# Kernel optimization log

Measured on AMD Instinct MI355X. Metric: run time of the kernel, lower is better.

The kernel has to match this reference:

```python
import jax, jax.numpy as jnp
import numpy as np

A = 16          # n_agents
H = 128         # rnn_hidden_dim
IN = 128        # input_shape
NA = 32         # n_attention
NACT = 14       # n_actions
TAU = 0.5       # gumbel_softmax_tau
B_ENV = 1024    # parallel envs
BZ = B_ENV * A

# neighbor index: for agent i, all j != i (matches select_ind in torch code)
IDX = np.array([[j for j in range(A) if j != i] for i in range(A)])  # [A, A-1]


def gru_cell(x, h, Wih, Whh, bih, bhh):
    # torch GRUCell gate order: r, z, n
    gi = x @ Wih.T + bih
    gh = h @ Whh.T + bhh
    ir, iz, inn = jnp.split(gi, 3, axis=-1)
    hr, hz, hn = jnp.split(gh, 3, axis=-1)
    r = jax.nn.sigmoid(ir + hr)
    z = jax.nn.sigmoid(iz + hz)
    n = jnp.tanh(inn + r * hn)
    return (1.0 - z) * n + z * h


def run_gru(seq, Wih, Whh, bih, bhh):
    # seq: [T, N, D]; returns all hidden states [T, N, H]
    h0 = jnp.zeros((seq.shape[1], Whh.shape[1]), seq.dtype)
    def step(h, x):
        h2 = gru_cell(x, h, Wih, Whh, bih, bhh)
        return h2, h2
    _, ys = jax.lax.scan(step, h0, seq)
    return ys


def setup_inputs() -> dict:
    key = jax.random.key(0)
    ks = jax.random.split(key, 24)
    def u(k, shape, fan):
        s = 1.0 / np.sqrt(fan)
        return jax.random.uniform(k, shape, jnp.float32, -s, s)
    inp = {
        "inputs": jax.random.normal(ks[0], (BZ, IN), jnp.float32),
        "hidden_state": jax.random.normal(ks[1], (BZ, H), jnp.float32),
        "gumbel_u": jax.random.uniform(ks[2], (BZ * (A - 1), 2), jnp.float32),
        # fc1
        "W1": u(ks[3], (H, IN), IN), "b1": u(ks[4], (H,), IN),
        # GRUCell
        "Wih_c": u(ks[5], (3 * H, H), H), "Whh_c": u(ks[6], (3 * H, H), H),
        "bih_c": u(ks[7], (3 * H,), H), "bhh_c": u(ks[8], (3 * H,), H),
        # bi-GRU forward dir (input 2H)
        "Wih_f": u(ks[9], (3 * H, 2 * H), H), "Whh_f": u(ks[10], (3 * H, H), H),
        "bih_f": u(ks[11], (3 * H,), H), "bhh_f": u(ks[12], (3 * H,), H),
        # bi-GRU backward dir
        "Wih_b": u(ks[13], (3 * H, 2 * H), H), "Whh_b": u(ks[14], (3 * H, H), H),
        "bih_b": u(ks[15], (3 * H,), H), "bhh_b": u(ks[16], (3 * H,), H),
        # hard classifier
        "Wc": u(ks[17], (2, 2 * H), 2 * H), "bc": u(ks[18], (2,), 2 * H),
        # attention projections (no bias)
        "Wq": u(ks[19], (NA, H), H), "Wk": u(ks[20], (NA, H), H),
        # fc2
        "W2": u(ks[21], (NACT, 2 * H), 2 * H), "b2": u(ks[22], (NACT,), 2 * H),
    }
    return inp


def reference(inputs, hidden_state, gumbel_u, W1, b1, Wih_c, Whh_c, bih_c, bhh_c,
              Wih_f, Whh_f, bih_f, bhh_f, Wih_b, Whh_b, bih_b, bhh_b,
              Wc, bc, Wq, Wk, W2, b2):
    bz = inputs.shape[0]
    B = bz // A
    x1 = jax.nn.relu(inputs @ W1.T + b1)
    h_rnn = gru_cell(x1, hidden_state.reshape(-1, H), Wih_c, Whh_c, bih_c, bhh_c)  # [bz, H]

    h3 = h_rnn.reshape(B, A, H)
    nbr = h3[:, IDX, :]                                           # [B, A, A-1, H]
    self_rep = jnp.broadcast_to(h3[:, :, None, :], (B, A, A - 1, H))
    pairs = jnp.concatenate([self_rep, nbr], axis=-1)             # [B, A, A-1, 2H]
    seq = pairs.transpose(2, 0, 1, 3).reshape(A - 1, bz, 2 * H)   # [T, bz, 2H]

    yf = run_gru(seq, Wih_f, Whh_f, bih_f, bhh_f)
    yb = jnp.flip(run_gru(jnp.flip(seq, 0), Wih_b, Whh_b, bih_b, bhh_b), 0)
    h_hard = jnp.concatenate([yf, yb], axis=-1)                   # [T, bz, 2H]
    h_hard = h_hard.transpose(1, 0, 2).reshape(-1, 2 * H)         # [bz*T, 2H]

    logits = h_hard @ Wc.T + bc                                   # [bz*T, 2]
    g = -jnp.log(-jnp.log(gumbel_u + 1e-10) + 1e-10)
    gs = jax.nn.softmax((logits + g) / TAU, axis=-1)
    hard_w = gs[:, 1].reshape(B, A, A - 1)                        # hard gate

    q = (h_rnn @ Wq.T).reshape(B, A, NA)
    k = (h_rnn @ Wk.T).reshape(B, A, NA)
    kn = k[:, IDX, :] * hard_w[..., None]                         # [B, A, A-1, NA]
    scores = jnp.einsum('bad,bamd->bam', q, kn) / np.sqrt(NA)
    soft_w = jax.nn.softmax(scores, axis=-1)                      # [B, A, A-1]

    w = hard_w * soft_w
    agg = jnp.einsum('bam,bamh->bah', w, nbr).reshape(bz, H)
    out = jnp.concatenate([h_rnn, agg], axis=-1) @ W2.T + b2      # [bz, n_actions]
    return out, h_rnn
```

## Files before the change

### kernel.cpp

```cpp
#include <hip/hip_runtime.h>
#include <hip/hip_bf16.h>


typedef __attribute__((ext_vector_type(8))) short short8;
typedef __attribute__((ext_vector_type(4))) short short4v;
typedef __attribute__((ext_vector_type(4))) float float4v;

#define BF2F(x) __bfloat162float(x)
typedef __hip_bfloat16 bf;

__device__ __forceinline__ float frcp(float x) {
  return __builtin_amdgcn_rcpf(x);
}
__device__ __forceinline__ float fsigmoid(float x) {
  return frcp(1.f + __expf(-x));
}
__device__ __forceinline__ float ftanh(float x) {
  float e = __expf(2.f * x);
  return 1.f - 2.f * frcp(1.f + e);
}
__device__ __forceinline__ float rdv(const void* p, int i, int f) {
  return f ? ((const float*)p)[i] : BF2F(((const bf*)p)[i]);
}

static const int AO[23] = {
  0, 2097152, 4194304, 4685824, 4702208, 4702336, 4751488, 4800640, 4801024,
  4801408, 4899712, 4948864, 4949248, 4949632, 5047936, 5097088, 5097472,
  5097856, 5098368, 5098384, 5102480, 5106576, 5110160};
static const int AN[23] = {
  2097152, 2097152, 491520, 16384, 128, 49152, 49152, 384, 384, 98304, 49152,
  384, 384, 98304, 49152, 384, 384, 512, 2, 4096, 4096, 3584, 14};

struct CArgs {
  const void* src[23];
  int n[23];
  int off[23];
};

__global__ void kConvert(CArgs a, int* __restrict__ flagOut,
                         bf* __restrict__ arena,
                         const void* __restrict__ WqR, const void* __restrict__ WkR,
                         const void* __restrict__ W2R, const void* __restrict__ WcR,
                         bf* __restrict__ Wqk, bf* __restrict__ W2p,
                         bf* __restrict__ Wcb) {
  __shared__ int sflag;
  if (threadIdx.x == 0) sflag = 0;
  __syncthreads();
  {
    const unsigned short* p0 = (const unsigned short*)a.src[0];
    int hit = 0;
    for (int i = threadIdx.x; i < 4096; i += 256) {
      int e = (p0[i] >> 7) & 0xFF;
      if (e >= 0xC0) hit = 1;
    }
    if (hit) atomicOr(&sflag, 1);
  }
  __syncthreads();
  const int f = sflag;
  const int b = blockIdx.y;
  if (b == 0 && blockIdx.x == 0 && threadIdx.x == 0) *flagOut = f;

  if (b == 23) {
    int idx = blockIdx.x * 256 + threadIdx.x;
    if (idx < 8192) {
      int r = idx >> 7, c = idx & 127;
      float v = (r < 32) ? rdv(WqR, r * 128 + c, f) : rdv(WkR, (r - 32) * 128 + c, f);
      Wqk[idx] = __float2bfloat16(v);
    }
    if (idx < 4096)
      W2p[idx] = __float2bfloat16((idx < 3584) ? rdv(W2R, idx, f) : 0.f);
    if (idx < 512) {
      int dir = idx >> 8, l = (idx >> 7) & 1, k = idx & 127;
      Wcb[idx] = __float2bfloat16(rdv(WcR, l * 256 + dir * 128 + k, f));
    }
    return;
  }
  if (b == 2 || b == 18 || b == 22) return;
  const int n = a.n[b];
  const int nv = n & ~7;
  bf* dst = arena + a.off[b];
  const int gid = blockIdx.x * 256 + threadIdx.x;
  const int gs = gridDim.x * 256;
  if (f) {
    const float* s = (const float*)a.src[b];
    for (int i = gid * 8; i < nv; i += gs * 8) {
      float4 x0 = *(const float4*)(s + i);
      float4 x1 = *(const float4*)(s + i + 4);
      short8 v;
      bf t;
      t = __float2bfloat16(x0.x); v[0] = *(short*)&t;
      t = __float2bfloat16(x0.y); v[1] = *(short*)&t;
      t = __float2bfloat16(x0.z); v[2] = *(short*)&t;
      t = __float2bfloat16(x0.w); v[3] = *(short*)&t;
      t = __float2bfloat16(x1.x); v[4] = *(short*)&t;
      t = __float2bfloat16(x1.y); v[5] = *(short*)&t;
      t = __float2bfloat16(x1.z); v[6] = *(short*)&t;
      t = __float2bfloat16(x1.w); v[7] = *(short*)&t;
      *(short8*)(dst + i) = v;
    }
    for (int i = nv + gid; i < n; i += gs) dst[i] = __float2bfloat16(s[i]);
  } else {
    const short8* s = (const short8*)a.src[b];
    short8* d = (short8*)dst;
    for (int i = gid; i * 8 < nv; i += gs) d[i] = s[i];
    const unsigned short* ss = (const unsigned short*)a.src[b];
    unsigned short* ds = (unsigned short*)dst;
    for (int i = nv + gid; i < n; i += gs) ds[i] = ss[i];
  }
}

__global__ __launch_bounds__(256) void kFused12(
    const bf* __restrict__ inputs, const bf* __restrict__ W1,
    const bf* __restrict__ b1, const bf* __restrict__ Wih,
    const bf* __restrict__ bih, bf* __restrict__ gi) {
  __shared__ bf sX[16][136];
  const int tid = threadIdx.x;
  const int wave = tid >> 6, lane = tid & 63;
  const int quad = lane >> 4, ci = lane & 15;
  const int row0 = blockIdx.x * 16;

  float4v xa[2];
#pragma unroll
  for (int i = 0; i < 2; ++i) xa[i] = {0.f, 0.f, 0.f, 0.f};
#pragma unroll
  for (int ks = 0; ks < 4; ++ks) {
    short8 inr = *(const short8*)(inputs + (size_t)(row0 + ci) * 128 + ks * 32 + quad * 8);
#pragma unroll
    for (int c2 = 0; c2 < 2; ++c2) {
      int ct = wave * 2 + c2;
      short8 wfr = *(const short8*)(W1 + (size_t)(ct * 16 + ci) * 128 + ks * 32 + quad * 8);
      xa[c2] = __builtin_amdgcn_mfma_f32_16x16x32_bf16(wfr, inr, xa[c2], 0, 0, 0);
    }
  }
#pragma unroll
  for (int c2 = 0; c2 < 2; ++c2) {
    int ct = wave * 2 + c2;
    short4v v4;
#pragma unroll
    for (int r = 0; r < 4; ++r) {
      float v = xa[c2][r] + BF2F(b1[ct * 16 + quad * 4 + r]);
      v = fmaxf(v, 0.f);
      bf t = __float2bfloat16(v);
      v4[r] = *(short*)&t;
    }
    *(short4v*)&sX[ci][ct * 16 + quad * 4] = v4;
  }
  __syncthreads();

  short8 af[4];
#pragma unroll
  for (int ks = 0; ks < 4; ++ks)
    af[ks] = *(const short8*)&sX[ci][ks * 32 + quad * 8];

  float4v acc[6];
#pragma unroll
  for (int i = 0; i < 6; ++i) acc[i] = {0.f, 0.f, 0.f, 0.f};
#pragma unroll
  for (int ks = 0; ks < 4; ++ks)
#pragma unroll
    for (int j = 0; j < 6; ++j) {
      short8 b = *(const short8*)(Wih + (size_t)((wave * 6 + j) * 16 + ci) * 128 + ks * 32 + quad * 8);
      acc[j] = __builtin_amdgcn_mfma_f32_16x16x32_bf16(af[ks], b, acc[j], 0, 0, 0);
    }
#pragma unroll
  for (int j = 0; j < 6; ++j) {
    int col = (wave * 6 + j) * 16 + ci;
    float bv = BF2F(bih[col]);
#pragma unroll
    for (int r = 0; r < 4; ++r)
      gi[(size_t)(row0 + quad * 4 + r) * 384 + col] = __float2bfloat16(acc[j][r] + bv);
  }
}

__global__ __launch_bounds__(256, 4) void kStep(
    const bf* __restrict__ Hp, const bf* __restrict__ Whh,
    const bf* __restrict__ G, int gld,
    const bf* __restrict__ bhh,
    bf* __restrict__ Ho, float* __restrict__ HcopyF) {
  const int half = blockIdx.z;
  const int tid = threadIdx.x;
  const int wave = tid >> 6, lane = tid & 63;
  const int quad = lane >> 4, ci = lane & 15;
  const int mr = blockIdx.x * 32 + (wave & 1) * 16;
  const int nt0 = (wave >> 1) * 2;

  float4v acc[6];
#pragma unroll
  for (int i = 0; i < 6; ++i) acc[i] = {0.f, 0.f, 0.f, 0.f};

#pragma unroll
  for (int ks = 0; ks < 4; ++ks) {
    short8 a = *(const short8*)(Hp + (size_t)(mr + ci) * 128 + ks * 32 + quad * 8);
#pragma unroll
    for (int g = 0; g < 3; ++g)
#pragma unroll
      for (int nt = 0; nt < 2; ++nt) {
        short8 b = *(const short8*)(Whh + (size_t)(g * 128 + half * 64 + (nt0 + nt) * 16 + ci) * 128 + ks * 32 + quad * 8);
        acc[g * 2 + nt] = __builtin_amdgcn_mfma_f32_16x16x32_bf16(a, b, acc[g * 2 + nt], 0, 0, 0);
      }
  }

  float bR[2], bZ[2], bN[2];
#pragma unroll
  for (int nt = 0; nt < 2; ++nt) {
    int c = half * 64 + (nt0 + nt) * 16 + ci;
    bR[nt] = BF2F(bhh[c]);
    bZ[nt] = BF2F(bhh[128 + c]);
    bN[nt] = BF2F(bhh[256 + c]);
  }

#pragma unroll
  for (int r = 0; r < 4; ++r) {
    int rr = mr + quad * 4 + r;
    const bf* gs = G + (size_t)rr * gld;
#pragma unroll
    for (int nt = 0; nt < 2; ++nt) {
      int c = half * 64 + (nt0 + nt) * 16 + ci;
      float gr = BF2F(gs[c]), gz = BF2F(gs[128 + c]), gnn = BF2F(gs[256 + c]);
      float pre_r = acc[nt][r] + gr + bR[nt];
      float pre_z = acc[2 + nt][r] + gz + bZ[nt];
      float hn_   = acc[4 + nt][r] + bN[nt];
      float rg = fsigmoid(pre_r);
      float zg = fsigmoid(pre_z);
      float ng = ftanh(gnn + rg * hn_);
      float hp = BF2F(Hp[(size_t)rr * 128 + c]);
      float hv = ng + zg * (hp - ng);
      Ho[(size_t)rr * 128 + c] = __float2bfloat16(hv);
      if (HcopyF) HcopyF[(size_t)rr * 128 + c] = hv;
    }
  }
}

__global__ __launch_bounds__(512, 4) void kSeq(
    const bf* __restrict__ hrnn,
    const bf* __restrict__ Wih_f, const bf* __restrict__ Wih_b,
    const bf* __restrict__ Whh_f, const bf* __restrict__ Whh_b,
    const bf* __restrict__ bih_f, const bf* __restrict__ bih_b,
    const bf* __restrict__ bhh_f, const bf* __restrict__ bhh_b,
    const bf* __restrict__ Wcb, float* __restrict__ L) {
  __shared__ float sGiN[16][3][132];
  __shared__ bf sH[2][16][136];
  __shared__ float sL[16][15][2];
  __shared__ bf sWc[2][136];

  const int env = blockIdx.x;
  const int dir = blockIdx.y;
  const int tid = threadIdx.x;
  const int wave = tid >> 6, lane = tid & 63;
  const int nh = wave;
  const int quad = lane >> 4, ci = lane & 15;
  const bf* Wih = dir ? Wih_b : Wih_f;
  const bf* Whh = dir ? Whh_b : Whh_f;
  const bf* bih = dir ? bih_b : bih_f;
  const bf* bhh = dir ? bhh_b : bhh_f;
  const int h0q = nh * 16 + quad * 4;

  float4v gS[3], gN[3];
#pragma unroll
  for (int i = 0; i < 3; ++i) { gS[i] = {0.f, 0.f, 0.f, 0.f}; gN[i] = {0.f, 0.f, 0.f, 0.f}; }
#pragma unroll
  for (int ks = 0; ks < 4; ++ks) {
    short8 bh = *(const short8*)(hrnn + (size_t)(env * 16 + ci) * 128 + ks * 32 + quad * 8);
#pragma unroll
    for (int g = 0; g < 3; ++g) {
      const bf* wrow = Wih + (size_t)(g * 128 + nh * 16 + ci) * 256 + ks * 32 + quad * 8;
      short8 ws = *(const short8*)(wrow);
      short8 wn = *(const short8*)(wrow + 128);
      gS[g] = __builtin_amdgcn_mfma_f32_16x16x32_bf16(ws, bh, gS[g], 0, 0, 0);
      gN[g] = __builtin_amdgcn_mfma_f32_16x16x32_bf16(wn, bh, gN[g], 0, 0, 0);
    }
  }
#pragma unroll
  for (int g = 0; g < 3; ++g)
#pragma unroll
    for (int r = 0; r < 4; ++r) {
      int c = g * 128 + h0q + r;
      float bv = BF2F(bih[c]);
      if (g < 2) bv += BF2F(bhh[c]);
      gS[g][r] += bv;
    }
#pragma unroll
  for (int g = 0; g < 3; ++g)
    *(float4v*)&sGiN[ci][g][h0q] = gN[g];

  {
    bf z = __float2bfloat16(0.f);
    bf* p = &sH[0][0][0];
    for (int i = tid; i < 16 * 136; i += 512) p[i] = z;
    if (tid < 256)
      sWc[tid >> 7][tid & 127] = Wcb[(dir * 2 + (tid >> 7)) * 128 + (tid & 127)];
  }

  short8 Bf[12];
#pragma unroll
  for (int g = 0; g < 3; ++g)
#pragma unroll
    for (int ks = 0; ks < 4; ++ks)
      Bf[g * 4 + ks] =
          *(const short8*)(Whh + (size_t)(g * 128 + nh * 16 + ci) * 128 + ks * 32 + quad * 8);

  float bNc[4];
#pragma unroll
  for (int r = 0; r < 4; ++r) bNc[r] = BF2F(bhh[256 + h0q + r]);

  float hPrev[4];
#pragma unroll
  for (int r = 0; r < 4; ++r) hPrev[r] = 0.f;

  __syncthreads();

  for (int t = 0; t < 15; ++t) {
    const int cur = t & 1, nxt = cur ^ 1;
    const int m = dir ? (14 - t) : t;
    const int jr = m + ((m >= ci) ? 1 : 0);

    float4v nbR = *(const float4v*)&sGiN[jr][0][h0q];
    float4v nbZ = *(const float4v*)&sGiN[jr][1][h0q];
    float4v nbN = *(const float4v*)&sGiN[jr][2][h0q];

    float4v acc[3];
#pragma unroll
    for (int i = 0; i < 3; ++i) acc[i] = {0.f, 0.f, 0.f, 0.f};
    float4v lacc = {0.f, 0.f, 0.f, 0.f};
#pragma unroll
    for (int ks = 0; ks < 4; ++ks) {
      short8 bh = *(const short8*)&sH[cur][ci][ks * 32 + quad * 8];
#pragma unroll
      for (int g = 0; g < 3; ++g)
        acc[g] = __builtin_amdgcn_mfma_f32_16x16x32_bf16(Bf[g * 4 + ks], bh, acc[g], 0, 0, 0);
      if (nh == 0) {
        short8 wv = *(const short8*)&sWc[ci & 1][ks * 32 + quad * 8];
        lacc = __builtin_amdgcn_mfma_f32_16x16x32_bf16(wv, bh, lacc, 0, 0, 0);
      }
    }
    if (nh == 0 && t > 0 && quad == 0) {
      int mp = dir ? (15 - t) : (t - 1);
      sL[ci][mp][0] = lacc[0];
      sL[ci][mp][1] = lacc[1];
    }

    short4v hv4;
#pragma unroll
    for (int r = 0; r < 4; ++r) {
      float pre_r = acc[0][r] + gS[0][r] + nbR[r];
      float pre_z = acc[1][r] + gS[1][r] + nbZ[r];
      float gnn   = gS[2][r] + nbN[r];
      float hn_   = acc[2][r] + bNc[r];
      float rg = fsigmoid(pre_r);
      float zg = fsigmoid(pre_z);
      float ng = ftanh(gnn + rg * hn_);
      float hv = ng + zg * (hPrev[r] - ng);
      hPrev[r] = hv;
      bf b = __float2bfloat16(hv);
      hv4[r] = *(short*)&b;
    }
    *(short4v*)&sH[nxt][ci][h0q] = hv4;
    __syncthreads();
  }

  if (nh == 0) {
    float4v lacc = {0.f, 0.f, 0.f, 0.f};
#pragma unroll
    for (int ks = 0; ks < 4; ++ks) {
      short8 bh = *(const short8*)&sH[1][ci][ks * 32 + quad * 8];
      short8 wv = *(const short8*)&sWc[ci & 1][ks * 32 + quad * 8];
      lacc = __builtin_amdgcn_mfma_f32_16x16x32_bf16(wv, bh, lacc, 0, 0, 0);
    }
    if (quad == 0) {
      int mf = dir ? 0 : 14;
      sL[ci][mf][0] = lacc[0];
      sL[ci][mf][1] = lacc[1];
    }
  }
  __syncthreads();

  {
    float* Ld = L + (size_t)dir * 491520 + (size_t)env * 480;
    for (int i = tid; i < 480; i += 512) {
      int row = i / 30, rem = i - row * 30;
      int mm = rem >> 1, l = rem & 1;
      Ld[i] = sL[row][mm][l];
    }
  }
}

__global__ __launch_bounds__(256) void kTail(
    const bf* __restrict__ h, const bf* __restrict__ Wqk,
    const float* __restrict__ L, const void* __restrict__ guRaw,
    const void* __restrict__ bcRaw, const int* __restrict__ flag,
    const bf* __restrict__ W2p, const void* __restrict__ b2Raw,
    float* __restrict__ out) {
  __shared__ float sh[16 * 132];
  __shared__ float sqk[16 * 64];
  __shared__ float shw[240];
  __shared__ float sw[16 * 16];
  __shared__ bf sAgg[16][136];
  const int bb = blockIdx.x;
  const int tid = threadIdx.x;
  const int f = *flag;
  const int a = tid >> 4, i = tid & 15;

  {
    const int w = tid >> 6, lane = tid & 63;
    const int quad = lane >> 4, ci = lane & 15;
    float4v acc = {0.f, 0.f, 0.f, 0.f};
#pragma unroll
    for (int ks = 0; ks < 4; ++ks) {
      short8 a_ = *(const short8*)(h + (size_t)(bb * 16 + ci) * 128 + ks * 32 + quad * 8);
      short8 b_ = *(const short8*)(Wqk + (size_t)(w * 16 + ci) * 128 + ks * 32 + quad * 8);
      acc = __builtin_amdgcn_mfma_f32_16x16x32_bf16(a_, b_, acc, 0, 0, 0);
    }
#pragma unroll
    for (int r = 0; r < 4; ++r)
      sqk[(quad * 4 + r) * 64 + w * 16 + ci] = acc[r];
  }
  for (int k = tid; k < 2048; k += 256)
    sh[(k >> 7) * 132 + (k & 127)] = BF2F(h[(size_t)bb * 2048 + k]);
  if (tid < 240) {
    int idx = bb * 240 + tid;
    float l0 = L[(size_t)idx * 2]     + L[491520 + (size_t)idx * 2]     + rdv(bcRaw, 0, f);
    float l1 = L[(size_t)idx * 2 + 1] + L[491520 + (size_t)idx * 2 + 1] + rdv(bcRaw, 1, f);
    float u0 = rdv(guRaw, idx * 2, f);
    float u1 = rdv(guRaw, idx * 2 + 1, f);
    float g0 = -__logf(-__logf(u0 + 1e-10f) + 1e-10f);
    float g1 = -__logf(-__logf(u1 + 1e-10f) + 1e-10f);
    shw[tid] = fsigmoid(((l1 + g1) - (l0 + g0)) * 2.0f);
  }
  __syncthreads();

  float s = -1e30f;
  if (i < 15) {
    int j = i + (i >= a);
    float d = 0.f;
#pragma unroll
    for (int c = 0; c < 32; ++c) d += sqk[a * 64 + c] * sqk[j * 64 + 32 + c];
    s = shw[a * 15 + i] * d * 0.17677669529663687f;
  }
  float mx = s;
#pragma unroll
  for (int d = 1; d < 16; d <<= 1) mx = fmaxf(mx, __shfl_xor(mx, d));
  float ex = (i < 15) ? __expf(s - mx) : 0.f;
  float sum = ex;
#pragma unroll
  for (int d = 1; d < 16; d <<= 1) sum += __shfl_xor(sum, d);
  float w = (i < 15) ? (ex * frcp(sum)) * shw[a * 15 + i] : 0.f;
  sw[a * 16 + i] = w;
  __syncthreads();

  float ac[8] = {0, 0, 0, 0, 0, 0, 0, 0};
  for (int mm = 0; mm < 15; ++mm) {
    int jm = mm + (mm >= a);
    float wm = sw[a * 16 + mm];
    const float* shp = &sh[jm * 132 + i * 8];
    float4 h0 = *(const float4*)shp;
    float4 h1 = *(const float4*)(shp + 4);
    ac[0] += wm * h0.x; ac[1] += wm * h0.y; ac[2] += wm * h0.z; ac[3] += wm * h0.w;
    ac[4] += wm * h1.x; ac[5] += wm * h1.y; ac[6] += wm * h1.z; ac[7] += wm * h1.w;
  }
  short8 v;
#pragma unroll
  for (int d = 0; d < 8; ++d) {
    bf b = __float2bfloat16(ac[d]);
    v[d] = *(short*)&b;
  }
  *(short8*)&sAgg[a][i * 8] = v;
  __syncthreads();

  if (tid < 64) {
    const int quad = tid >> 4, ci = tid & 15;
    const int mr = bb * 16;
    float4v acc = {0.f, 0.f, 0.f, 0.f};
#pragma unroll
    for (int ks = 0; ks < 4; ++ks) {
      short8 a_ = *(const short8*)(h + (size_t)(mr + ci) * 128 + ks * 32 + quad * 8);
      short8 b_ = *(const short8*)(W2p + (size_t)ci * 256 + ks * 32 + quad * 8);
      acc = __builtin_amdgcn_mfma_f32_16x16x32_bf16(a_, b_, acc, 0, 0, 0);
    }
#pragma unroll
    for (int ks = 0; ks < 4; ++ks) {
      short8 a_ = *(const short8*)&sAgg[ci][ks * 32 + quad * 8];
      short8 b_ = *(const short8*)(W2p + (size_t)ci * 256 + 128 + ks * 32 + quad * 8);
      acc = __builtin_amdgcn_mfma_f32_16x16x32_bf16(a_, b_, acc, 0, 0, 0);
    }
    if (ci < 14) {
      float bv = rdv(b2Raw, ci, f);
#pragma unroll
      for (int r = 0; r < 4; ++r)
        out[(size_t)(mr + quad * 4 + r) * 14 + ci] = acc[r] + bv;
    }
  }
}

extern "C" void kernel_launch(void* const* d_in, const int* in_sizes, int n_in,
                              void* d_out, int out_size, void* d_ws, size_t ws_size,
                              hipStream_t stream) {
  const size_t OFF_ARENA = 0;
  const size_t OFF_FLAG  = 10220544;
  const size_t OFF_A     = 10220800;
  const size_t OFF_WQK   = 26998016;
  const size_t OFF_WCB   = 27014400;
  const size_t OFF_W2P   = 27410944;
  const size_t OFF_HRNN  = 27419136;
  const size_t NEEDED    = 84042240;
  if (ws_size < NEEDED) return;
  if (n_in < 23 || in_sizes[0] != 2097152 || in_sizes[3] != 16384 ||
      in_sizes[5] != 49152 || in_sizes[9] != 98304 || in_sizes[17] != 512 ||
      in_sizes[19] != 4096 || in_sizes[21] != 3584 || out_size != 2326528)
    return;

  char* ws = (char*)d_ws;
  bf*    arena = (bf*)(ws + OFF_ARENA);
  float* L     = (float*)(ws + OFF_ARENA);
  int*   flag  = (int*)(ws + OFF_FLAG);
  bf*    gi_c  = (bf*)(ws + OFF_A + 4194304);
  bf*    Wqk   = (bf*)(ws + OFF_WQK);
  bf*    Wcb   = (bf*)(ws + OFF_WCB);
  bf*    W2p   = (bf*)(ws + OFF_W2P);
  bf*    hrnn  = (bf*)(ws + OFF_HRNN);

  float* out14 = (float*)d_out;
  float* outh  = (float*)d_out + 229376;

  CArgs ca;
  for (int i = 0; i < 23; ++i) { ca.src[i] = d_in[i]; ca.n[i] = AN[i]; ca.off[i] = AO[i]; }
  kConvert<<<dim3(128, 24), 256, 0, stream>>>(ca, flag, arena,
                                              d_in[19], d_in[20], d_in[21], d_in[17],
                                              Wqk, W2p, Wcb);

  const bf* inputs = arena + AO[0];
  const bf* hidden = arena + AO[1];
  const bf* W1     = arena + AO[3];
  const bf* b1     = arena + AO[4];
  const bf* Wih_c  = arena + AO[5];
  const bf* Whh_c  = arena + AO[6];
  const bf* bih_c  = arena + AO[7];
  const bf* bhh_c  = arena + AO[8];
  const bf* Wih_f  = arena + AO[9];
  const bf* Whh_f  = arena + AO[10];
  const bf* bih_f  = arena + AO[11];
  const bf* bhh_f  = arena + AO[12];
  const bf* Wih_b  = arena + AO[13];
  const bf* Whh_b  = arena + AO[14];
  const bf* bih_b  = arena + AO[15];
  const bf* bhh_b  = arena + AO[16];

  kFused12<<<dim3(1024), 256, 0, stream>>>(inputs, W1, b1, Wih_c, bih_c, gi_c);
  kStep<<<dim3(512, 1, 2), 256, 0, stream>>>(hidden, Whh_c, gi_c, 384, bhh_c,
                                             hrnn, outh);
  kSeq<<<dim3(1024, 2), 512, 0, stream>>>(hrnn, Wih_f, Wih_b, Whh_f, Whh_b,
                                          bih_f, bih_b, bhh_f, bhh_b, Wcb, L);
  kTail<<<dim3(1024), 256, 0, stream>>>(hrnn, Wqk, L, d_in[2], d_in[18], flag,
                                        W2p, d_in[22], out14);
}
```

Baseline: 267.4 us.

## Fuse fc1, GRU input projection and GRU cell step into one kernel

Merges the fc1+Wih kernel and the GRUCell step kernel into a single kernel. Each block now computes both the input and hidden gate projections with MFMA and applies the gate math in registers. This removes the bf16 gi intermediate round trip through global memory and one kernel launch. Separately, the sequence kernel now seeds its MFMA accumulators with the precomputed gate and bias terms, saving a few adds per step. The fused kernel keeps twelve accumulators per wave instead of six, which raises register pressure.

```diff
diff --git a/kernel.cpp b/kernel.cpp
--- a/kernel.cpp
+++ b/kernel.cpp
@@ -109,10 +109,12 @@
   }
 }
 
-__global__ __launch_bounds__(256) void kFused12(
+__global__ __launch_bounds__(256) void kPre(
     const bf* __restrict__ inputs, const bf* __restrict__ W1,
     const bf* __restrict__ b1, const bf* __restrict__ Wih,
-    const bf* __restrict__ bih, bf* __restrict__ gi) {
+    const bf* __restrict__ bih, const bf* __restrict__ hidden,
+    const bf* __restrict__ Whh, const bf* __restrict__ bhh,
+    bf* __restrict__ hrnn, float* __restrict__ outh) {
   __shared__ bf sX[16][136];
   const int tid = threadIdx.x;
   const int wave = tid >> 6, lane = tid & 63;
@@ -152,81 +154,44 @@
   for (int ks = 0; ks < 4; ++ks)
     af[ks] = *(const short8*)&sX[ci][ks * 32 + quad * 8];
 
-  float4v acc[6];
-#pragma unroll
-  for (int i = 0; i < 6; ++i) acc[i] = {0.f, 0.f, 0.f, 0.f};
-#pragma unroll
-  for (int ks = 0; ks < 4; ++ks)
-#pragma unroll
-    for (int j = 0; j < 6; ++j) {
-      short8 b = *(const short8*)(Wih + (size_t)((wave * 6 + j) * 16 + ci) * 128 + ks * 32 + quad * 8);
-      acc[j] = __builtin_amdgcn_mfma_f32_16x16x32_bf16(af[ks], b, acc[j], 0, 0, 0);
-    }
-#pragma unroll
-  for (int j = 0; j < 6; ++j) {
-    int col = (wave * 6 + j) * 16 + ci;
-    float bv = BF2F(bih[col]);
-#pragma unroll
-    for (int r = 0; r < 4; ++r)
-      gi[(size_t)(row0 + quad * 4 + r) * 384 + col] = __float2bfloat16(acc[j][r] + bv);
-  }
-}
-
-__global__ __launch_bounds__(256, 4) void kStep(
-    const bf* __restrict__ Hp, const bf* __restrict__ Whh,
-    const bf* __restrict__ G, int gld,
-    const bf* __restrict__ bhh,
-    bf* __restrict__ Ho, float* __restrict__ HcopyF) {
-  const int half = blockIdx.z;
-  const int tid = threadIdx.x;
-  const int wave = tid >> 6, lane = tid & 63;
-  const int quad = lane >> 4, ci = lane & 15;
-  const int mr = blockIdx.x * 32 + (wave & 1) * 16;
-  const int nt0 = (wave >> 1) * 2;
-
-  float4v acc[6];
-#pragma unroll
-  for (int i = 0; i < 6; ++i) acc[i] = {0.f, 0.f, 0.f, 0.f};
-
+  float4v ah[6], ag[6];
+#pragma unroll
+  for (int i = 0; i < 6; ++i) { ah[i] = {0.f, 0.f, 0.f, 0.f}; ag[i] = {0.f, 0.f, 0.f, 0.f}; }
 #pragma unroll
   for (int ks = 0; ks < 4; ++ks) {
-    short8 a = *(const short8*)(Hp + (size_t)(mr + ci) * 128 + ks * 32 + quad * 8);
+    short8 hr = *(const short8*)(hidden + (size_t)(row0 + ci) * 128 + ks * 32 + quad * 8);
 #pragma unroll
     for (int g = 0; g < 3; ++g)
 #pragma unroll
       for (int nt = 0; nt < 2; ++nt) {
-        short8 b = *(const short8*)(Whh + (size_t)(g * 128 + half * 64 + (nt0 + nt) * 16 + ci) * 128 + ks * 32 + quad * 8);
-        acc[g * 2 + nt] = __builtin_amdgcn_mfma_f32_16x16x32_bf16(a, b, acc[g * 2 + nt], 0, 0, 0);
+        int wrow = g * 128 + wave * 32 + nt * 16 + ci;
+        short8 bw = *(const short8*)(Whh + (size_t)wrow * 128 + ks * 32 + quad * 8);
+        ah[g * 2 + nt] = __builtin_amdgcn_mfma_f32_16x16x32_bf16(hr, bw, ah[g * 2 + nt], 0, 0, 0);
+        short8 bi_ = *(const short8*)(Wih + (size_t)wrow * 128 + ks * 32 + quad * 8);
+        ag[g * 2 + nt] = __builtin_amdgcn_mfma_f32_16x16x32_bf16(af[ks], bi_, ag[g * 2 + nt], 0, 0, 0);
       }
   }
 
-  float bR[2], bZ[2], bN[2];
 #pragma unroll
   for (int nt = 0; nt < 2; ++nt) {
-    int c = half * 64 + (nt0 + nt) * 16 + ci;
-    bR[nt] = BF2F(bhh[c]);
-    bZ[nt] = BF2F(bhh[128 + c]);
-    bN[nt] = BF2F(bhh[256 + c]);
-  }
-
-#pragma unroll
-  for (int r = 0; r < 4; ++r) {
-    int rr = mr + quad * 4 + r;
-    const bf* gs = G + (size_t)rr * gld;
-#pragma unroll
-    for (int nt = 0; nt < 2; ++nt) {
-      int c = half * 64 + (nt0 + nt) * 16 + ci;
-      float gr = BF2F(gs[c]), gz = BF2F(gs[128 + c]), gnn = BF2F(gs[256 + c]);
-      float pre_r = acc[nt][r] + gr + bR[nt];
-      float pre_z = acc[2 + nt][r] + gz + bZ[nt];
-      float hn_   = acc[4 + nt][r] + bN[nt];
+    int c = wave * 32 + nt * 16 + ci;
+    float biR = BF2F(bih[c]),       bhR = BF2F(bhh[c]);
+    float biZ = BF2F(bih[128 + c]), bhZ = BF2F(bhh[128 + c]);
+    float biN = BF2F(bih[256 + c]), bhN = BF2F(bhh[256 + c]);
+#pragma unroll
+    for (int r = 0; r < 4; ++r) {
+      int rr = row0 + quad * 4 + r;
+      float pre_r = ah[nt][r] + (ag[nt][r] + biR) + bhR;
+      float pre_z = ah[2 + nt][r] + (ag[2 + nt][r] + biZ) + bhZ;
+      float gnn   = ag[4 + nt][r] + biN;
+      float hn_   = ah[4 + nt][r] + bhN;
       float rg = fsigmoid(pre_r);
       float zg = fsigmoid(pre_z);
       float ng = ftanh(gnn + rg * hn_);
-      float hp = BF2F(Hp[(size_t)rr * 128 + c]);
+      float hp = BF2F(hidden[(size_t)rr * 128 + c]);
       float hv = ng + zg * (hp - ng);
-      Ho[(size_t)rr * 128 + c] = __float2bfloat16(hv);
-      if (HcopyF) HcopyF[(size_t)rr * 128 + c] = hv;
+      hrnn[(size_t)rr * 128 + c] = __float2bfloat16(hv);
+      outh[(size_t)rr * 128 + c] = hv;
     }
   }
 }
@@ -299,9 +264,9 @@
       Bf[g * 4 + ks] =
           *(const short8*)(Whh + (size_t)(g * 128 + nh * 16 + ci) * 128 + ks * 32 + quad * 8);
 
-  float bNc[4];
-#pragma unroll
-  for (int r = 0; r < 4; ++r) bNc[r] = BF2F(bhh[256 + h0q + r]);
+  float4v bNcV;
+#pragma unroll
+  for (int r = 0; r < 4; ++r) bNcV[r] = BF2F(bhh[256 + h0q + r]);
 
   float hPrev[4];
 #pragma unroll
@@ -319,8 +284,9 @@
     float4v nbN = *(const float4v*)&sGiN[jr][2][h0q];
 
     float4v acc[3];
-#pragma unroll
-    for (int i = 0; i < 3; ++i) acc[i] = {0.f, 0.f, 0.f, 0.f};
+    acc[0] = gS[0];
+    acc[1] = gS[1];
+    acc[2] = bNcV;
     float4v lacc = {0.f, 0.f, 0.f, 0.f};
 #pragma unroll
     for (int ks = 0; ks < 4; ++ks) {
@@ -342,10 +308,10 @@
     short4v hv4;
 #pragma unroll
     for (int r = 0; r < 4; ++r) {
-      float pre_r = acc[0][r] + gS[0][r] + nbR[r];
-      float pre_z = acc[1][r] + gS[1][r] + nbZ[r];
+      float pre_r = acc[0][r] + nbR[r];
+      float pre_z = acc[1][r] + nbZ[r];
       float gnn   = gS[2][r] + nbN[r];
-      float hn_   = acc[2][r] + bNc[r];
+      float hn_   = acc[2][r];
       float rg = fsigmoid(pre_r);
       float zg = fsigmoid(pre_z);
       float ng = ftanh(gnn + rg * hn_);
@@ -496,7 +462,6 @@
                               hipStream_t stream) {
   const size_t OFF_ARENA = 0;
   const size_t OFF_FLAG  = 10220544;
-  const size_t OFF_A     = 10220800;
   const size_t OFF_WQK   = 26998016;
   const size_t OFF_WCB   = 27014400;
   const size_t OFF_W2P   = 27410944;
@@ -512,7 +477,6 @@
   bf*    arena = (bf*)(ws + OFF_ARENA);
   float* L     = (float*)(ws + OFF_ARENA);
   int*   flag  = (int*)(ws + OFF_FLAG);
-  bf*    gi_c  = (bf*)(ws + OFF_A + 4194304);
   bf*    Wqk   = (bf*)(ws + OFF_WQK);
   bf*    Wcb   = (bf*)(ws + OFF_WCB);
   bf*    W2p   = (bf*)(ws + OFF_W2P);
@@ -544,9 +508,8 @@
   const bf* bih_b  = arena + AO[15];
   const bf* bhh_b  = arena + AO[16];
 
-  kFused12<<<dim3(1024), 256, 0, stream>>>(inputs, W1, b1, Wih_c, bih_c, gi_c);
-  kStep<<<dim3(512, 1, 2), 256, 0, stream>>>(hidden, Whh_c, gi_c, 384, bhh_c,
-                                             hrnn, outh);
+  kPre<<<dim3(1024), 256, 0, stream>>>(inputs, W1, b1, Wih_c, bih_c, hidden,
+                                       Whh_c, bhh_c, hrnn, outh);
   kSeq<<<dim3(1024, 2), 512, 0, stream>>>(hrnn, Wih_f, Wih_b, Whh_f, Whh_b,
                                           bih_f, bih_b, bhh_f, bhh_b, Wcb, L);
   kTail<<<dim3(1024), 256, 0, stream>>>(hrnn, Wqk, L, d_in[2], d_in[18], flag,
```

Result: no change. 264.6 us (-1.0%).
